# Optimization experiments

Measured on AMD Instinct MI355X. Metric: run time of the kernel, lower is better.

The kernel has to match this reference:

```python
import jax, jax.numpy as jnp
import numpy as np

EMBED_DIM = 768
OUT_DIM = 768
EPS = 1e-06


def setup_inputs() -> dict:
    key = jax.random.key(0)
    ks = jax.random.split(key, 7)
    s_in = 1.0 / np.sqrt(EMBED_DIM)
    x = jax.random.normal(ks[0], (32, 1024, EMBED_DIM), dtype=jnp.float32)
    Wq = jax.random.normal(ks[1], (OUT_DIM, EMBED_DIM), dtype=jnp.float32) * s_in
    bq = jax.random.normal(ks[2], (OUT_DIM,), dtype=jnp.float32) * 0.01
    Wk = jax.random.normal(ks[3], (OUT_DIM, EMBED_DIM), dtype=jnp.float32) * s_in
    bk = jax.random.normal(ks[4], (OUT_DIM,), dtype=jnp.float32) * 0.01
    Wv = jax.random.normal(ks[5], (OUT_DIM, EMBED_DIM), dtype=jnp.float32) * s_in
    bv = jax.random.normal(ks[6], (OUT_DIM,), dtype=jnp.float32) * 0.01
    return {"x": x, "Wq": Wq, "bq": bq, "Wk": Wk, "bk": bk, "Wv": Wv, "bv": bv}


def reference(x, Wq, bq, Wk, bk, Wv, bv):
    # Q/K/V projections: nn.Linear computes x @ W.T + b
    Q = jnp.einsum('bnd,od->bno', x, Wq) + bq  # [B, N, O]
    K = jnp.einsum('bnd,od->bno', x, Wk) + bk
    V = jnp.einsum('bnd,od->bno', x, Wv) + bv
    scale = jnp.sqrt(jnp.asarray(OUT_DIM, dtype=x.dtype)) + EPS
    attn = jnp.einsum('bqo,bko->bqk', Q, K) / scale  # [B, N, N]
    weights = jax.nn.softmax(attn, axis=-1)
    # dropout p=0.0 -> identity (eval/inference)
    return jnp.einsum('bqk,bko->bqo', weights, V)
```

## Files before the change

kernel.cpp:

```cpp
#include <hip/hip_runtime.h>
#include <hip/hip_bf16.h>


typedef float  floatx4  __attribute__((ext_vector_type(4)));
typedef float  floatx16 __attribute__((ext_vector_type(16)));
typedef short  short8   __attribute__((ext_vector_type(8)));

#define LOG2E 1.44269504088896f

__device__ __forceinline__ unsigned cvtpk(float lo, float hi) {
    unsigned r;
    asm("v_cvt_pk_bf16_f32 %0, %1, %2" : "=v"(r) : "v"(lo), "v"(hi));
    return r;
}
__device__ __forceinline__ floatx16 mfma32(short8 a, short8 b, floatx16 c) {
    return __builtin_amdgcn_mfma_f32_32x32x16_bf16(a, b, c, 0, 0, 0);
}
__device__ __forceinline__ void load_lds16(const void* g, void* lds) {
    __builtin_amdgcn_global_load_lds(
        (const __attribute__((address_space(1))) unsigned int*)g,
        (__attribute__((address_space(3))) unsigned int*)lds, 16, 0, 0);
}
__device__ __forceinline__ void bar_lds() {
    asm volatile("s_waitcnt lgkmcnt(0)" ::: "memory");
    __builtin_amdgcn_s_barrier();
    __builtin_amdgcn_sched_barrier(0);
}
__device__ __forceinline__ void bar_vm() {
    asm volatile("s_waitcnt vmcnt(0)" ::: "memory");
    __builtin_amdgcn_s_barrier();
    __builtin_amdgcn_sched_barrier(0);
}

__global__ __launch_bounds__(256) void cvt_bf16(
    const float* __restrict__ s0, unsigned short* __restrict__ d0, int n0,
    const float* __restrict__ s1, unsigned short* __restrict__ d1, int n1,
    const float* __restrict__ s2, unsigned short* __restrict__ d2, int n2,
    const float* __restrict__ W,  unsigned short* __restrict__ Wf)
{
    if (blockIdx.x >= 2048) {
        const int i = (blockIdx.x - 2048) * 256 + threadIdx.x;
        const int o  = i / 96;
        const int d0i = (i % 96) * 8;
        const floatx4* s = (const floatx4*)(W + (size_t)o * 768 + d0i);
        floatx4 v0 = s[0], v1 = s[1];
        uint4 st;
        st.x = cvtpk(v0[0], v0[1]);
        st.y = cvtpk(v0[2], v0[3]);
        st.z = cvtpk(v1[0], v1[1]);
        st.w = cvtpk(v1[2], v1[3]);
        const size_t idx = (((size_t)(o >> 5) * 48 + (d0i >> 4)) * 64
                            + ((o & 31) | (((d0i >> 3) & 1) << 5))) * 8;
        *reinterpret_cast<uint4*>(Wf + idx) = st;
        return;
    }
    const int stride = 2048 * 256;
    const int base   = blockIdx.x * 256 + threadIdx.x;
    const float* ss[3] = {s0, s1, s2};
    unsigned short* dd[3] = {d0, d1, d2};
    const int nn[3] = {n0, n1, n2};
#pragma unroll
    for (int j = 0; j < 3; ++j) {
        const floatx4* s = (const floatx4*)ss[j];
        uint4* d = (uint4*)dd[j];
        for (int i = base; i < nn[j]; i += stride) {
            floatx4 v0 = s[2 * i];
            floatx4 v1 = s[2 * i + 1];
            uint4 o;
            o.x = cvtpk(v0[0], v0[1]);
            o.y = cvtpk(v0[2], v0[3]);
            o.z = cvtpk(v1[0], v1[1]);
            o.w = cvtpk(v1[2], v1[3]);
            d[i] = o;
        }
    }
}

template <int MODE>
__global__ __launch_bounds__(256, 2) void gemm_lds(
    const unsigned short* __restrict__ A,
    const unsigned short* __restrict__ B,
    unsigned short* __restrict__ C, const float* __restrict__ bias,
    float alpha)
{
    __shared__ __align__(16) unsigned short As[2][128 * 64];
    __shared__ __align__(16) unsigned short Bs[2][128 * 64];

    const int tid = threadIdx.x;
    const int l   = tid & 63;
    const int w   = tid >> 6;
    const int wr  = w >> 1;
    const int wc  = w & 1;
    const int lo5 = l & 31;
    const int hi  = l >> 5;

    const int bid = blockIdx.x;
    const int swz = (bid & 7) * 192 + (bid >> 3);
    const int i0  = (MODE == 0 ? (swz % 6) : (swz / 6)) * 128;
    const int j0  = (MODE == 0 ? (swz / 6) : (swz % 6)) * 128;

    const int srow = l >> 3;
    const int sc16 = (l & 7) ^ srow;
    const unsigned short* Ag = A + (size_t)(i0 + srow) * 768 + sc16 * 8;
    const unsigned short* Bg = B + (size_t)(j0 + srow) * 768 + sc16 * 8;

    floatx16 acc[2][2] = {};

    auto STAGE = [&](int buf, int kt) {
        const int k0 = kt * 64;
#pragma unroll
        for (int t4 = 0; t4 < 4; ++t4) {
            const int t = w * 4 + t4;
            load_lds16(Ag + (size_t)t * 8 * 768 + k0, &As[buf][t * 512]);
            load_lds16(Bg + (size_t)t * 8 * 768 + k0, &Bs[buf][t * 512]);
        }
    };
    auto COMPUTE = [&](int buf) {
        const char* Ab = (const char*)As[buf];
        const char* Bb = (const char*)Bs[buf];
#pragma unroll
        for (int kk = 0; kk < 4; ++kk) {
            short8 a[2], b[2];
#pragma unroll
            for (int i = 0; i < 2; ++i) {
                const int r = wr * 64 + i * 32 + lo5;
                const unsigned off = r * 128 + ((unsigned)((kk * 2 + hi) ^ (r & 7)) << 4);
                a[i] = *reinterpret_cast<const short8*>(Ab + off);
            }
#pragma unroll
            for (int j = 0; j < 2; ++j) {
                const int r = wc * 64 + j * 32 + lo5;
                const unsigned off = r * 128 + ((unsigned)((kk * 2 + hi) ^ (r & 7)) << 4);
                b[j] = *reinterpret_cast<const short8*>(Bb + off);
            }
#pragma unroll
            for (int i = 0; i < 2; ++i)
#pragma unroll
                for (int j = 0; j < 2; ++j)
                    acc[i][j] = mfma32(a[i], b[j], acc[i][j]);
        }
    };

    STAGE(0, 0);
    __syncthreads();
#pragma unroll 1
    for (int kt = 0; kt < 12; ++kt) {
        if (kt + 1 < 12) STAGE((kt + 1) & 1, kt + 1);
        COMPUTE(kt & 1);
        __syncthreads();
    }

#pragma unroll
    for (int i = 0; i < 2; ++i) {
        float bvv[16];
        if (MODE == 0) {
#pragma unroll
            for (int r = 0; r < 16; ++r) {
                const int ol = (r & 3) + 8 * (r >> 2) + 4 * hi;
                bvv[r] = bias[i0 + wr * 64 + i * 32 + ol];
            }
        }
#pragma unroll
        for (int j = 0; j < 2; ++j) {
            float bj = 0.f;
            if (MODE == 1) bj = bias[j0 + wc * 64 + j * 32 + lo5];
            float v[16];
#pragma unroll
            for (int r = 0; r < 16; ++r)
                v[r] = (MODE == 0) ? (acc[i][j][r] + bvv[r]) * alpha
                                   : (acc[i][j][r] + bj);
#pragma unroll
            for (int cc = 0; cc < 2; ++cc) {
                unsigned w0 = cvtpk(v[8 * cc + 0], v[8 * cc + 1]);
                unsigned w1 = cvtpk(v[8 * cc + 2], v[8 * cc + 3]);
                unsigned w2 = cvtpk(v[8 * cc + 4], v[8 * cc + 5]);
                unsigned w3 = cvtpk(v[8 * cc + 6], v[8 * cc + 7]);
                unsigned x0 = __shfl_xor(w0, 32);
                unsigned x1 = __shfl_xor(w1, 32);
                unsigned x2 = __shfl_xor(w2, 32);
                unsigned x3 = __shfl_xor(w3, 32);
                uint4 st;
                st.x = hi ? x2 : w0;
                st.y = hi ? x3 : w1;
                st.z = hi ? w2 : x0;
                st.w = hi ? w3 : x1;
                size_t idx;
                if (MODE == 0) {
                    const int og = i0 + wr * 64 + i * 32 + cc * 16;
                    const int mg = j0 + wc * 64 + j * 32 + lo5;
                    idx = ((size_t)(mg >> 5) * 48 + (og >> 4)) * 512
                        + (size_t)(lo5 | (hi << 5)) * 8;
                } else {
                    const int ng = i0 + wr * 64 + i * 32 + cc * 16;
                    const int dg = j0 + wc * 64 + j * 32 + lo5;
                    idx = ((size_t)(ng >> 4) * 24 + (dg >> 5)) * 512
                        + (size_t)(lo5 | (hi << 5)) * 8;
                }
                *reinterpret_cast<uint4*>(C + idx) = st;
            }
        }
    }
}

__global__ __launch_bounds__(512, 1) void attn_kernel(
    const unsigned short* __restrict__ Wqf,
    const unsigned short* __restrict__ Kf,
    const unsigned short* __restrict__ Vf,
    const float* __restrict__ x,
    const float* __restrict__ bq,
    float* __restrict__ out)
{
    __shared__ __align__(16) unsigned short Q_lds[96 * 512];
    __shared__ __align__(16) unsigned short P_lds[2][32 * 512];

    const int tid = threadIdx.x;
    const int l   = tid & 63;
    const int w   = tid >> 6;
    const int lo5 = l & 31;
    const int hi  = l >> 5;

    const int bid = blockIdx.x;
    const int xcd = bid & 7;
    const int jj  = bid >> 3;
    const int b   = (jj >> 4) * 8 + xcd;
    const int qi  = jj & 15;
    const int q0  = qi * 64;

    const float MFIX2 = 12.0f * LOG2E;
    const float alpha = LOG2E / (sqrtf(768.0f) + 1e-6f);

    const short8* Kp = reinterpret_cast<const short8*>(Kf)
                       + ((size_t)b * 32 * 48) * 64 + l;
    const short8* Vp = reinterpret_cast<const short8*>(Vf)
                       + ((size_t)b * 64 * 24) * 64 + l;

    floatx16 acc6[6] = {};
    short8 kbuf[8], vbuf[4][3];

    {
        float* Xs0 = (float*)P_lds[0];
        float* Xs1 = (float*)P_lds[1];
        const float* xg = x + (size_t)(b * 1024 + q0) * 768;
        const short8* Wp = reinterpret_cast<const short8*>(Wqf) + l;

        const int c16 = tid & 31;
        const int r0  = tid >> 5;

        auto XSTAGE = [&](int p, float* Xs) {
#pragma unroll
            for (int it = 0; it < 4; ++it) {
                const int row = it * 16 + r0;
                const int u   = it * 512 + tid;
                load_lds16(xg + (size_t)row * 768 + p * 128 + ((c16 ^ (row & 7)) << 2),
                           &Xs[u * 4]);
            }
        };

        XSTAGE(0, Xs0);
        bar_vm();

        short8 wbuf2[2][3];
#pragma unroll 1
        for (int p = 0; p < 6; ++p) {
            float* Xs = (p & 1) ? Xs1 : Xs0;
#pragma unroll
            for (int jo = 0; jo < 3; ++jo)
                wbuf2[0][jo] = Wp[(size_t)((w * 3 + jo) * 48 + p * 8) * 64];
            if (p + 1 < 6) XSTAGE(p + 1, (p & 1) ? Xs0 : Xs1);
#pragma unroll
            for (int it = 0; it < 8; ++it) {
                const int ks = p * 8 + it;
                if (it + 1 < 8) {
#pragma unroll
                    for (int jo = 0; jo < 3; ++jo)
                        wbuf2[(it + 1) & 1][jo] =
                            Wp[(size_t)((w * 3 + jo) * 48 + ks + 1) * 64];
                }
                short8 xf[2];
#pragma unroll
                for (int jq = 0; jq < 2; ++jq) {
                    const int row = jq * 32 + lo5;
                    const int un  = it * 4 + hi * 2;
                    floatx4 f0 = *reinterpret_cast<const floatx4*>(
                        &Xs[((row << 5) + ((un + 0) ^ (row & 7))) * 4]);
                    floatx4 f1 = *reinterpret_cast<const floatx4*>(
                        &Xs[((row << 5) + ((un + 1) ^ (row & 7))) * 4]);
                    uint4 u4;
                    u4.x = cvtpk(f0[0], f0[1]);
                    u4.y = cvtpk(f0[2], f0[3]);
                    u4.z = cvtpk(f1[0], f1[1]);
                    u4.w = cvtpk(f1[2], f1[3]);
                    xf[jq] = __builtin_bit_cast(short8, u4);
                }
                __builtin_amdgcn_s_setprio(1);
#pragma unroll
                for (int jo = 0; jo < 3; ++jo) {
#pragma unroll
                    for (int jq = 0; jq < 2; ++jq)
                        acc6[jo * 2 + jq] = mfma32(wbuf2[it & 1][jo], xf[jq],
                                                   acc6[jo * 2 + jq]);
                }
                __builtin_amdgcn_s_setprio(0);
            }
            bar_vm();
        }

        {
            const short8* Kc0 = Kp + (size_t)w * 48 * 64;
#pragma unroll
            for (int u = 0; u < 8; ++u) kbuf[u] = Kc0[(size_t)u * 64];
        }

#pragma unroll
        for (int jo = 0; jo < 3; ++jo) {
            const int o32 = w * 96 + jo * 32;
            float bvv[16];
#pragma unroll
            for (int r = 0; r < 16; ++r)
                bvv[r] = bq[o32 + (r & 3) + 8 * (r >> 2) + 4 * hi];
#pragma unroll
            for (int jq = 0; jq < 2; ++jq) {
                float v[16];
#pragma unroll
                for (int r = 0; r < 16; ++r)
                    v[r] = (acc6[jo * 2 + jq][r] + bvv[r]) * alpha;
#pragma unroll
                for (int cc = 0; cc < 2; ++cc) {
                    unsigned w0 = cvtpk(v[8 * cc + 0], v[8 * cc + 1]);
                    unsigned w1 = cvtpk(v[8 * cc + 2], v[8 * cc + 3]);
                    unsigned w2 = cvtpk(v[8 * cc + 4], v[8 * cc + 5]);
                    unsigned w3 = cvtpk(v[8 * cc + 6], v[8 * cc + 7]);
                    unsigned x0 = __shfl_xor(w0, 32);
                    unsigned x1 = __shfl_xor(w1, 32);
                    unsigned x2 = __shfl_xor(w2, 32);
                    unsigned x3 = __shfl_xor(w3, 32);
                    uint4 st;
                    st.x = hi ? x2 : w0;
                    st.y = hi ? x3 : w1;
                    st.z = hi ? w2 : x0;
                    st.w = hi ? w3 : x1;
                    const int ks_t = w * 6 + jo * 2 + cc;
                    *reinterpret_cast<uint4*>(
                        &Q_lds[((ks_t * 2 + jq) * 64 + (lo5 | (hi << 5))) * 8]) = st;
                }
            }
        }
    }
    bar_lds();

#pragma unroll
    for (int i = 0; i < 6; ++i) acc6[i] = (floatx16){};

    float l_reg0 = 0.f, l_reg1 = 0.f;

#pragma unroll 1
    for (int c = 0; c < 4; ++c) {
        floatx16 s0 = {}, s1 = {};
        const short8* Kc = Kp + (size_t)(c * 8 + w) * 48 * 64;
        short8 qa0 = *reinterpret_cast<const short8*>(&Q_lds[(0 * 64 + l) * 8]);
        short8 qa1 = *reinterpret_cast<const short8*>(&Q_lds[(1 * 64 + l) * 8]);
#pragma unroll 1
        for (int ks8 = 0; ks8 < 6; ++ks8) {
#pragma unroll
            for (int u = 0; u < 8; ++u) {
                const int ks = ks8 * 8 + u;
                short8 ka = kbuf[u];
                if (ks + 8 < 48) kbuf[u] = Kc[(size_t)(ks + 8) * 64];
                short8 qn0, qn1;
                if (ks + 1 < 48) {
                    qn0 = *reinterpret_cast<const short8*>(&Q_lds[(((ks + 1) * 2 + 0) * 64 + l) * 8]);
                    qn1 = *reinterpret_cast<const short8*>(&Q_lds[(((ks + 1) * 2 + 1) * 64 + l) * 8]);
                }
                __builtin_amdgcn_s_setprio(1);
                s0 = mfma32(ka, qa0, s0);
                s1 = mfma32(ka, qa1, s1);
                __builtin_amdgcn_s_setprio(0);
                qa0 = qn0;
                qa1 = qn1;
            }
        }

        const short8* Vc = Vp + (size_t)(c * 16) * 24 * 64;
#pragma unroll
        for (int g = 0; g < 4; ++g)
#pragma unroll
            for (int jv = 0; jv < 3; ++jv)
                vbuf[g][jv] = Vc[((size_t)g * 24 + w * 3 + jv) * 64];

        if (c < 3) {
            const short8* Kn = Kp + (size_t)((c + 1) * 8 + w) * 48 * 64;
#pragma unroll
            for (int u = 0; u < 8; ++u) kbuf[u] = Kn[(size_t)u * 64];
        }

        float p0[16], p1[16];
        float sum0 = 0.f, sum1 = 0.f;
#pragma unroll
        for (int r = 0; r < 16; ++r) {
            p0[r] = exp2f(s0[r] - MFIX2); sum0 += p0[r];
            p1[r] = exp2f(s1[r] - MFIX2); sum1 += p1[r];
        }
        l_reg0 += sum0 + __shfl_xor(sum0, 32);
        l_reg1 += sum1 + __shfl_xor(sum1, 32);

        char* Pb = (char*)P_lds[c & 1];
#pragma unroll
        for (int cc = 0; cc < 2; ++cc) {
#pragma unroll
            for (int jt = 0; jt < 2; ++jt) {
                const float* p = jt ? p1 : p0;
                unsigned w0 = cvtpk(p[8 * cc + 0], p[8 * cc + 1]);
                unsigned w1 = cvtpk(p[8 * cc + 2], p[8 * cc + 3]);
                unsigned w2 = cvtpk(p[8 * cc + 4], p[8 * cc + 5]);
                unsigned w3 = cvtpk(p[8 * cc + 6], p[8 * cc + 7]);
                unsigned x0 = __shfl_xor(w0, 32);
                unsigned x1 = __shfl_xor(w1, 32);
                unsigned x2 = __shfl_xor(w2, 32);
                unsigned x3 = __shfl_xor(w3, 32);
                uint4 st;
                st.x = hi ? x2 : w0;
                st.y = hi ? x3 : w1;
                st.z = hi ? w2 : x0;
                st.w = hi ? w3 : x1;
                const unsigned off = (((unsigned)(w * 2 + cc) * 2 + jt) * 64 + l) * 16;
                *reinterpret_cast<uint4*>(Pb + off) = st;
            }
        }
        bar_lds();

        short8 pa0 = *reinterpret_cast<const short8*>(Pb + ((0 * 64 + l) * 16));
        short8 pa1 = *reinterpret_cast<const short8*>(Pb + ((1 * 64 + l) * 16));
#pragma unroll
        for (int g = 0; g < 16; ++g) {
            short8 pn0, pn1;
            if (g + 1 < 16) {
                pn0 = *reinterpret_cast<const short8*>(Pb + ((((g + 1) * 2 + 0) * 64 + l) * 16));
                pn1 = *reinterpret_cast<const short8*>(Pb + ((((g + 1) * 2 + 1) * 64 + l) * 16));
            }
            short8 v0 = vbuf[g & 3][0];
            short8 v1 = vbuf[g & 3][1];
            short8 v2 = vbuf[g & 3][2];
            if (g < 12) {
#pragma unroll
                for (int jv = 0; jv < 3; ++jv)
                    vbuf[g & 3][jv] = Vc[((size_t)(g + 4) * 24 + w * 3 + jv) * 64];
            }
            __builtin_amdgcn_s_setprio(1);
            acc6[0] = mfma32(pa0, v0, acc6[0]);
            acc6[3] = mfma32(pa1, v0, acc6[3]);
            acc6[1] = mfma32(pa0, v1, acc6[1]);
            acc6[4] = mfma32(pa1, v1, acc6[4]);
            acc6[2] = mfma32(pa0, v2, acc6[2]);
            acc6[5] = mfma32(pa1, v2, acc6[5]);
            __builtin_amdgcn_s_setprio(0);
            pa0 = pn0;
            pa1 = pn1;
        }
    }

    bar_lds();
    float* lred = (float*)Q_lds;
    if (hi == 0) {
        lred[(w * 2 + 0) * 32 + lo5] = l_reg0;
        lred[(w * 2 + 1) * 32 + lo5] = l_reg1;
    }
    bar_lds();
    float lt0 = 0.f, lt1 = 0.f;
#pragma unroll
    for (int wv = 0; wv < 8; ++wv) {
        lt0 += lred[(wv * 2 + 0) * 32 + lo5];
        lt1 += lred[(wv * 2 + 1) * 32 + lo5];
    }
    const float li0 = 1.0f / lt0;
    const float li1 = 1.0f / lt1;

#pragma unroll
    for (int jt = 0; jt < 2; ++jt)
#pragma unroll
        for (int r = 0; r < 16; ++r) {
            const int qr = (r & 3) + 8 * (r >> 2) + 4 * hi;
            const float linv = __shfl(jt ? li1 : li0, qr);
            const size_t grow = (size_t)(b * 1024 + q0 + jt * 32 + qr) * 768;
#pragma unroll
            for (int jv = 0; jv < 3; ++jv)
                out[grow + (w * 3 + jv) * 32 + lo5] = acc6[jt * 3 + jv][r] * linv;
        }
}

extern "C" void kernel_launch(void* const* d_in, const int* in_sizes, int n_in,
                              void* d_out, int out_size, void* d_ws, size_t ws_size,
                              hipStream_t stream) {
    const float* x  = (const float*)d_in[0];
    const float* Wq = (const float*)d_in[1];
    const float* bq = (const float*)d_in[2];
    const float* Wk = (const float*)d_in[3];
    const float* bk = (const float*)d_in[4];
    const float* Wv = (const float*)d_in[5];
    const float* bv = (const float*)d_in[6];
    float* out = (float*)d_out;

    unsigned short* Wqf = (unsigned short*)d_ws;
    unsigned short* Kf  = (unsigned short*)d_ws + 25165824u;
    unsigned short* Vf  = (unsigned short*)d_ws + 50331648u;

    unsigned short* xb  = (unsigned short*)d_out;
    unsigned short* Wkb = (unsigned short*)d_out + 25165824u;
    unsigned short* Wvb = Wkb + 589824u;

    cvt_bf16<<<2336, 256, 0, stream>>>(x, xb, 3145728,
                                       Wk, Wkb, 73728,
                                       Wv, Wvb, 73728,
                                       Wq, Wqf);

    gemm_lds<0><<<1536, 256, 0, stream>>>(Wkb, xb, Kf, bk, 1.0f);
    gemm_lds<1><<<1536, 256, 0, stream>>>(xb, Wvb, Vf, bv, 1.0f);

    attn_kernel<<<dim3(512), 512, 0, stream>>>(Wqf, Kf, Vf, x, bq, out);
}
```

Baseline: 290.9 us.

## Stage bf16 x in attention Q-projection and convert fp32 Wq in-kernel

The fused attention kernel's Q projection now stages the pre-converted bf16 copy of x through LDS instead of fp32 x, which halves LDS staging bytes and removes the per-tile x conversion. In exchange, it reads fp32 Wq directly from global memory and converts it to bf16 in registers, so the separate Wq pre-pack pass in the conversion kernel is dropped. bf16 x now lives in the workspace rather than in the output buffer, so the attention kernel can read it safely. The cost is doubled global traffic for Wq per block (fp32, non-packed layout, strided rows) plus conversion work in the MFMA loop.

```diff
diff --git a/kernel.cpp b/kernel.cpp
--- a/kernel.cpp
+++ b/kernel.cpp
@@ -35,25 +35,8 @@
 __global__ __launch_bounds__(256) void cvt_bf16(
     const float* __restrict__ s0, unsigned short* __restrict__ d0, int n0,
     const float* __restrict__ s1, unsigned short* __restrict__ d1, int n1,
-    const float* __restrict__ s2, unsigned short* __restrict__ d2, int n2,
-    const float* __restrict__ W,  unsigned short* __restrict__ Wf)
+    const float* __restrict__ s2, unsigned short* __restrict__ d2, int n2)
 {
-    if (blockIdx.x >= 2048) {
-        const int i = (blockIdx.x - 2048) * 256 + threadIdx.x;
-        const int o  = i / 96;
-        const int d0i = (i % 96) * 8;
-        const floatx4* s = (const floatx4*)(W + (size_t)o * 768 + d0i);
-        floatx4 v0 = s[0], v1 = s[1];
-        uint4 st;
-        st.x = cvtpk(v0[0], v0[1]);
-        st.y = cvtpk(v0[2], v0[3]);
-        st.z = cvtpk(v1[0], v1[1]);
-        st.w = cvtpk(v1[2], v1[3]);
-        const size_t idx = (((size_t)(o >> 5) * 48 + (d0i >> 4)) * 64
-                            + ((o & 31) | (((d0i >> 3) & 1) << 5))) * 8;
-        *reinterpret_cast<uint4*>(Wf + idx) = st;
-        return;
-    }
     const int stride = 2048 * 256;
     const int base   = blockIdx.x * 256 + threadIdx.x;
     const float* ss[3] = {s0, s1, s2};
@@ -203,10 +186,10 @@
 }
 
 __global__ __launch_bounds__(512, 1) void attn_kernel(
-    const unsigned short* __restrict__ Wqf,
     const unsigned short* __restrict__ Kf,
     const unsigned short* __restrict__ Vf,
-    const float* __restrict__ x,
+    const unsigned short* __restrict__ xb,
+    const float* __restrict__ Wq,
     const float* __restrict__ bq,
     float* __restrict__ out)
 {
@@ -238,67 +221,67 @@
     short8 kbuf[8], vbuf[4][3];
 
     {
-        float* Xs0 = (float*)P_lds[0];
-        float* Xs1 = (float*)P_lds[1];
-        const float* xg = x + (size_t)(b * 1024 + q0) * 768;
-        const short8* Wp = reinterpret_cast<const short8*>(Wqf) + l;
-
-        const int c16 = tid & 31;
-        const int r0  = tid >> 5;
-
-        auto XSTAGE = [&](int p, float* Xs) {
+        unsigned short* Xs0 = P_lds[0];
+        unsigned short* Xs1 = P_lds[1];
+        const unsigned short* xg = xb + (size_t)(b * 1024 + q0) * 768;
+
+        auto XSTAGE = [&](int p, unsigned short* Xs) {
 #pragma unroll
             for (int it = 0; it < 4; ++it) {
-                const int row = it * 16 + r0;
                 const int u   = it * 512 + tid;
-                load_lds16(xg + (size_t)row * 768 + p * 128 + ((c16 ^ (row & 7)) << 2),
-                           &Xs[u * 4]);
+                const int row = u >> 5;
+                const int c16 = u & 31;
+                load_lds16(xg + (size_t)row * 768 + p * 256 + ((c16 ^ (row & 7)) << 3),
+                           &Xs[u * 8]);
             }
         };
 
         XSTAGE(0, Xs0);
         bar_vm();
 
-        short8 wbuf2[2][3];
+        floatx4 wf[2][3][2];
 #pragma unroll 1
-        for (int p = 0; p < 6; ++p) {
-            float* Xs = (p & 1) ? Xs1 : Xs0;
-#pragma unroll
-            for (int jo = 0; jo < 3; ++jo)
-                wbuf2[0][jo] = Wp[(size_t)((w * 3 + jo) * 48 + p * 8) * 64];
-            if (p + 1 < 6) XSTAGE(p + 1, (p & 1) ? Xs0 : Xs1);
-#pragma unroll
-            for (int it = 0; it < 8; ++it) {
-                const int ks = p * 8 + it;
-                if (it + 1 < 8) {
-#pragma unroll
-                    for (int jo = 0; jo < 3; ++jo)
-                        wbuf2[(it + 1) & 1][jo] =
-                            Wp[(size_t)((w * 3 + jo) * 48 + ks + 1) * 64];
+        for (int p = 0; p < 3; ++p) {
+            unsigned short* Xs = (p & 1) ? Xs1 : Xs0;
+#pragma unroll
+            for (int jo = 0; jo < 3; ++jo) {
+                const float* wp = Wq + (size_t)((w * 3 + jo) * 32 + lo5) * 768
+                                  + (p * 16) * 16 + hi * 8;
+                wf[0][jo][0] = *reinterpret_cast<const floatx4*>(wp);
+                wf[0][jo][1] = *reinterpret_cast<const floatx4*>(wp + 4);
+            }
+            if (p + 1 < 3) XSTAGE(p + 1, (p & 1) ? Xs0 : Xs1);
+#pragma unroll
+            for (int it = 0; it < 16; ++it) {
+                const int ks = p * 16 + it;
+                if (it + 1 < 16) {
+#pragma unroll
+                    for (int jo = 0; jo < 3; ++jo) {
+                        const float* wp = Wq + (size_t)((w * 3 + jo) * 32 + lo5) * 768
+                                          + (ks + 1) * 16 + hi * 8;
+                        wf[(it + 1) & 1][jo][0] = *reinterpret_cast<const floatx4*>(wp);
+                        wf[(it + 1) & 1][jo][1] = *reinterpret_cast<const floatx4*>(wp + 4);
+                    }
                 }
                 short8 xf[2];
 #pragma unroll
                 for (int jq = 0; jq < 2; ++jq) {
-                    const int row = jq * 32 + lo5;
-                    const int un  = it * 4 + hi * 2;
-                    floatx4 f0 = *reinterpret_cast<const floatx4*>(
-                        &Xs[((row << 5) + ((un + 0) ^ (row & 7))) * 4]);
-                    floatx4 f1 = *reinterpret_cast<const floatx4*>(
-                        &Xs[((row << 5) + ((un + 1) ^ (row & 7))) * 4]);
-                    uint4 u4;
-                    u4.x = cvtpk(f0[0], f0[1]);
-                    u4.y = cvtpk(f0[2], f0[3]);
-                    u4.z = cvtpk(f1[0], f1[1]);
-                    u4.w = cvtpk(f1[2], f1[3]);
-                    xf[jq] = __builtin_bit_cast(short8, u4);
+                    const int row  = jq * 32 + lo5;
+                    const int unit = (it * 2 + hi) ^ (row & 7);
+                    xf[jq] = *reinterpret_cast<const short8*>(&Xs[row * 256 + unit * 8]);
                 }
                 __builtin_amdgcn_s_setprio(1);
 #pragma unroll
                 for (int jo = 0; jo < 3; ++jo) {
+                    uint4 u4;
+                    u4.x = cvtpk(wf[it & 1][jo][0][0], wf[it & 1][jo][0][1]);
+                    u4.y = cvtpk(wf[it & 1][jo][0][2], wf[it & 1][jo][0][3]);
+                    u4.z = cvtpk(wf[it & 1][jo][1][0], wf[it & 1][jo][1][1]);
+                    u4.w = cvtpk(wf[it & 1][jo][1][2], wf[it & 1][jo][1][3]);
+                    short8 wa = __builtin_bit_cast(short8, u4);
 #pragma unroll
                     for (int jq = 0; jq < 2; ++jq)
-                        acc6[jo * 2 + jq] = mfma32(wbuf2[it & 1][jo], xf[jq],
-                                                   acc6[jo * 2 + jq]);
+                        acc6[jo * 2 + jq] = mfma32(wa, xf[jq], acc6[jo * 2 + jq]);
                 }
                 __builtin_amdgcn_s_setprio(0);
             }
@@ -499,21 +482,19 @@
     const float* bv = (const float*)d_in[6];
     float* out = (float*)d_out;
 
-    unsigned short* Wqf = (unsigned short*)d_ws;
-    unsigned short* Kf  = (unsigned short*)d_ws + 25165824u;
-    unsigned short* Vf  = (unsigned short*)d_ws + 50331648u;
-
-    unsigned short* xb  = (unsigned short*)d_out;
+    unsigned short* xb = (unsigned short*)d_ws;
+    unsigned short* Kf = xb + 25165824u;
+    unsigned short* Vf = xb + 50331648u;
+
     unsigned short* Wkb = (unsigned short*)d_out + 25165824u;
     unsigned short* Wvb = Wkb + 589824u;
 
-    cvt_bf16<<<2336, 256, 0, stream>>>(x, xb, 3145728,
+    cvt_bf16<<<2048, 256, 0, stream>>>(x, xb, 3145728,
                                        Wk, Wkb, 73728,
-                                       Wv, Wvb, 73728,
-                                       Wq, Wqf);
+                                       Wv, Wvb, 73728);
 
     gemm_lds<0><<<1536, 256, 0, stream>>>(Wkb, xb, Kf, bk, 1.0f);
     gemm_lds<1><<<1536, 256, 0, stream>>>(xb, Wvb, Vf, bv, 1.0f);
 
-    attn_kernel<<<dim3(512), 512, 0, stream>>>(Wqf, Kf, Vf, x, bq, out);
-}
+    attn_kernel<<<dim3(512), 512, 0, stream>>>(Kf, Vf, xb, Wq, bq, out);
+}
```

Measured after the change: 377.3 us. +29.7%, slower.
